# Kernel optimization log

Hardware: AMD Instinct MI355X
Metric: run time of the kernel (lower is better)

Reference implementation:

```python
import jax, jax.numpy as jnp
import numpy as np
import math

EPS = 1.1920929e-07  # torch F.rms_norm default eps = fp32 machine epsilon


def rms_norm(x):
    # normalize over last dim, no learned weight (matches F.rms_norm(x, (d,)))
    var = jnp.mean(jnp.square(x), axis=-1, keepdims=True)
    return x * jax.lax.rsqrt(var + EPS)


def rotary(x, cos, sin):
    # x: (B, T, H, D); cos/sin: (T, D) -> broadcast over B, H
    d2 = x.shape[-1] // 2
    x1, x2 = x[..., :d2], x[..., d2:]
    rot = jnp.concatenate([-x2, x1], axis=-1)  # rotate_half
    c = cos[None, :, None, :]
    s = sin[None, :, None, :]
    return x * c + rot * s


def setup_inputs() -> dict:
    key = jax.random.key(0)
    ks = jax.random.split(key, 5)
    B, T, C, H = 2, 2048, 1024, 16
    D = C // H
    x = jax.random.normal(ks[0], (B, T, C), dtype=jnp.float32)
    # real RoPE tables (theta=10000), duplicated across the two halves
    inv_freq = 1.0 / (10000.0 ** (np.arange(0, D, 2, dtype=np.float32) / D))
    pos = np.arange(T, dtype=np.float32)
    freqs = np.outer(pos, inv_freq)            # (T, D/2)
    emb = np.concatenate([freqs, freqs], -1)   # (T, D)
    cos = jnp.asarray(np.cos(emb), dtype=jnp.float32)
    sin = jnp.asarray(np.sin(emb), dtype=jnp.float32)
    sc_in = 1.0 / math.sqrt(C)
    W_attn = jax.random.normal(ks[1], (C, 3 * C), dtype=jnp.float32) * sc_in
    b_attn = jax.random.normal(ks[2], (3 * C,), dtype=jnp.float32) * 0.02
    W_proj = jax.random.normal(ks[3], (C, C), dtype=jnp.float32) * sc_in
    b_proj = jax.random.normal(ks[4], (C,), dtype=jnp.float32) * 0.02
    return {"x": x, "cos": cos, "sin": sin, "W_attn": W_attn, "b_attn": b_attn,
            "W_proj": W_proj, "b_proj": b_proj}


def reference(x, cos, sin, W_attn, b_attn, W_proj, b_proj):
    B, T, C = x.shape
    H = 16
    D = C // H
    qkv = x @ W_attn + b_attn                         # (B, T, 3C)
    qkv = qkv.reshape(B, T, 3, H, D)                  # 'b t (a h d) -> ...'
    q, k, v = qkv[:, :, 0], qkv[:, :, 1], qkv[:, :, 2]  # (B, T, H, D)
    q, k = rms_norm(q), rms_norm(k)
    q = rotary(q, cos, sin)
    k = rotary(k, cos, sin)
    # causal SDPA, scale = 1/sqrt(D)
    scale = 1.0 / math.sqrt(D)
    scores = jnp.einsum('bthd,bshd->bhts', q, k) * scale  # (B, H, T, T)
    causal = jnp.tril(jnp.ones((T, T), dtype=bool))
    scores = jnp.where(causal[None, None], scores, jnp.finfo(scores.dtype).min)
    attn = jax.nn.softmax(scores, axis=-1)
    y = jnp.einsum('bhts,bshd->bthd', attn, v)            # (B, T, H, D)
    y = y.reshape(B, T, C)
    return y @ W_proj + b_proj
```

## Files before the change

kernel.cpp:

```cpp
#include <hip/hip_runtime.h>
#include <math.h>

#define EPSV 1.1920929e-07f

typedef __attribute__((ext_vector_type(8))) short short8;
typedef __attribute__((ext_vector_type(4))) float f32x4;

__device__ __forceinline__ float bf2f(unsigned short u) {
    union { unsigned int i; float f; } c; c.i = ((unsigned int)u) << 16; return c.f;
}
__device__ __forceinline__ unsigned short f2bf(float f) {
    union { float f; unsigned int i; } c; c.f = f;
    unsigned int r = c.i + 0x7FFFu + ((c.i >> 16) & 1u);
    return (unsigned short)(r >> 16);
}
__device__ __forceinline__ unsigned int pack_bf16_ru(float a, float b) {
    union { float f; unsigned int i; } ca, cb; ca.f = a; cb.f = b;
    return __builtin_amdgcn_perm(cb.i + 0x8000u, ca.i + 0x8000u, 0x07060302u);
}
__device__ __forceinline__ void async_lds16(const unsigned short* g, unsigned short* l) {
    __builtin_amdgcn_global_load_lds(
        (const __attribute__((address_space(1))) unsigned int*)g,
        (__attribute__((address_space(3))) unsigned int*)l, 16, 0, 0);
}

__global__ __launch_bounds__(256) void cast_bf16(
    const float* __restrict__ src, unsigned short* __restrict__ dst, int n)
{
    const int i = (blockIdx.x * 256 + threadIdx.x) * 4;
    if (i >= n) return;
    const float4 v = *(const float4*)&src[i];
    ushort4 o;
    o.x = f2bf(v.x); o.y = f2bf(v.y); o.z = f2bf(v.z); o.w = f2bf(v.w);
    *(ushort4*)&dst[i] = o;
}

__global__ __launch_bounds__(256) void transpose_cast_both(
    const float* __restrict__ Wa, unsigned short* __restrict__ Wat,
    const float* __restrict__ Wp, unsigned short* __restrict__ Wpt)
{
    __shared__ float tile[32][33];
    int bx = blockIdx.x;
    const float* W; unsigned short* Wt; int N;
    if (bx < 96) { W = Wa; Wt = Wat; N = 3072; }
    else         { W = Wp; Wt = Wpt; N = 1024; bx -= 96; }
    const int n0 = bx * 32, k0 = blockIdx.y * 32;
    const int r = threadIdx.x >> 3, c4 = (threadIdx.x & 7) * 4;
    const float4 v = *(const float4*)&W[(size_t)(k0 + r) * N + n0 + c4];
    tile[r][c4 + 0] = v.x; tile[r][c4 + 1] = v.y;
    tile[r][c4 + 2] = v.z; tile[r][c4 + 3] = v.w;
    __syncthreads();
    ushort4 o;
    o.x = f2bf(tile[c4 + 0][r]); o.y = f2bf(tile[c4 + 1][r]);
    o.z = f2bf(tile[c4 + 2][r]); o.w = f2bf(tile[c4 + 3][r]);
    *(ushort4*)&Wt[(size_t)(n0 + r) * 1024 + k0 + c4] = o;
}

template <bool OUT_BF16>
__global__ __launch_bounds__(256) void gemm_bf16(
    const unsigned short* __restrict__ A,
    const unsigned short* __restrict__ Bt,
    const float* __restrict__ bias,
    void* __restrict__ Cv,
    int M, int N, int K)
{
    __shared__ unsigned short As0[128][32], As1[128][32];
    __shared__ unsigned short Bs0[128][32], Bs1[128][32];
    const int t    = threadIdx.x;
    const int lane = t & 63;
    const int wv   = t >> 6;
    const int wrow = (wv >> 1) * 64;
    const int wcol = (wv & 1) * 64;
    const int m0 = blockIdx.y * 128;
    const int n0 = blockIdx.x * 128;
    const int col  = lane & 15;
    const int quad = lane >> 4;

    const int srow = (wv << 5) + (lane >> 2);
    const int scol = (lane & 3) << 3;
    const unsigned short* a00 = A  + (size_t)(m0 + srow) * K + scol;
    const unsigned short* a10 = a00 + (size_t)16 * K;
    const unsigned short* a01 = a00 + 32;
    const unsigned short* a11 = a10 + 32;
    const unsigned short* b00 = Bt + (size_t)(n0 + srow) * K + scol;
    const unsigned short* b10 = b00 + (size_t)16 * K;
    const unsigned short* b01 = b00 + 32;
    const unsigned short* b11 = b10 + 32;
    unsigned short* al0 = &As0[srow][scol];
    unsigned short* al1 = &As0[srow + 16][scol];
    unsigned short* al2 = &As1[srow][scol];
    unsigned short* al3 = &As1[srow + 16][scol];
    unsigned short* bl0 = &Bs0[srow][scol];
    unsigned short* bl1 = &Bs0[srow + 16][scol];
    unsigned short* bl2 = &Bs1[srow][scol];
    unsigned short* bl3 = &Bs1[srow + 16][scol];

    f32x4 acc[4][4];
    #pragma unroll
    for (int i = 0; i < 4; ++i)
        #pragma unroll
        for (int j = 0; j < 4; ++j)
            acc[i][j] = (f32x4){0.f, 0.f, 0.f, 0.f};

    for (int k0 = 0; k0 < K; k0 += 64) {
        async_lds16(a00, al0);
        async_lds16(a10, al1);
        async_lds16(a01, al2);
        async_lds16(a11, al3);
        async_lds16(b00, bl0);
        async_lds16(b10, bl1);
        async_lds16(b01, bl2);
        async_lds16(b11, bl3);
        a00 += 64; a10 += 64; a01 += 64; a11 += 64;
        b00 += 64; b10 += 64; b01 += 64; b11 += 64;
        __syncthreads();
        short8 af[2][4], bf[2][4];
        #pragma unroll
        for (int mt = 0; mt < 4; ++mt) {
            af[0][mt] = *(const short8*)&As0[wrow + mt * 16 + col][quad << 3];
            af[1][mt] = *(const short8*)&As1[wrow + mt * 16 + col][quad << 3];
        }
        #pragma unroll
        for (int nt = 0; nt < 4; ++nt) {
            bf[0][nt] = *(const short8*)&Bs0[wcol + nt * 16 + col][quad << 3];
            bf[1][nt] = *(const short8*)&Bs1[wcol + nt * 16 + col][quad << 3];
        }
        #pragma unroll
        for (int ks = 0; ks < 2; ++ks)
            #pragma unroll
            for (int mt = 0; mt < 4; ++mt)
                #pragma unroll
                for (int nt = 0; nt < 4; ++nt)
                    acc[mt][nt] = __builtin_amdgcn_mfma_f32_16x16x32_bf16(
                        af[ks][mt], bf[ks][nt], acc[mt][nt], 0, 0, 0);
        __syncthreads();
    }

    const int rowq = quad << 2;
    #pragma unroll
    for (int nt = 0; nt < 4; ++nt) {
        const int n = n0 + wcol + nt * 16 + col;
        const float bv = bias[n];
        #pragma unroll
        for (int mt = 0; mt < 4; ++mt) {
            #pragma unroll
            for (int r = 0; r < 4; ++r) {
                const int m = m0 + wrow + mt * 16 + rowq + r;
                const float v = acc[mt][nt][r] + bv;
                if (OUT_BF16)
                    ((unsigned short*)Cv)[(size_t)m * N + n] = f2bf(v);
                else
                    ((float*)Cv)[(size_t)m * N + n] = v;
            }
        }
    }
}

__global__ __launch_bounds__(256) void gemm_bf16_n64(
    const unsigned short* __restrict__ A,
    const unsigned short* __restrict__ Bt,
    const float* __restrict__ bias,
    float* __restrict__ C,
    int M, int N, int K)
{
    __shared__ unsigned short As0[128][32], As1[128][32];
    __shared__ unsigned short Bs0[64][32], Bs1[64][32];
    const int t    = threadIdx.x;
    const int lane = t & 63;
    const int wv   = t >> 6;
    const int wrow = wv << 5;
    const int m0 = blockIdx.y * 128;
    const int n0 = blockIdx.x * 64;
    const int col  = lane & 15;
    const int quad = lane >> 4;

    const int srow = (wv << 5) + (lane >> 2);
    const int scol = (lane & 3) << 3;
    const unsigned short* a00 = A  + (size_t)(m0 + srow) * K + scol;
    const unsigned short* a10 = a00 + (size_t)16 * K;
    const unsigned short* a01 = a00 + 32;
    const unsigned short* a11 = a10 + 32;
    const int bsrow = (wv << 4) + (lane >> 2);
    const unsigned short* b00 = Bt + (size_t)(n0 + bsrow) * K + scol;
    const unsigned short* b01 = b00 + 32;
    unsigned short* al0 = &As0[srow][scol];
    unsigned short* al1 = &As0[srow + 16][scol];
    unsigned short* al2 = &As1[srow][scol];
    unsigned short* al3 = &As1[srow + 16][scol];
    unsigned short* bl0 = &Bs0[bsrow][scol];
    unsigned short* bl1 = &Bs1[bsrow][scol];

    f32x4 acc[2][4];
    #pragma unroll
    for (int i = 0; i < 2; ++i)
        #pragma unroll
        for (int j = 0; j < 4; ++j)
            acc[i][j] = (f32x4){0.f, 0.f, 0.f, 0.f};

    for (int k0 = 0; k0 < K; k0 += 64) {
        async_lds16(a00, al0);
        async_lds16(a10, al1);
        async_lds16(a01, al2);
        async_lds16(a11, al3);
        async_lds16(b00, bl0);
        async_lds16(b01, bl1);
        a00 += 64; a10 += 64; a01 += 64; a11 += 64;
        b00 += 64; b01 += 64;
        __syncthreads();
        short8 af[2][2], bf[2][4];
        #pragma unroll
        for (int mt = 0; mt < 2; ++mt) {
            af[0][mt] = *(const short8*)&As0[wrow + mt * 16 + col][quad << 3];
            af[1][mt] = *(const short8*)&As1[wrow + mt * 16 + col][quad << 3];
        }
        #pragma unroll
        for (int nt = 0; nt < 4; ++nt) {
            bf[0][nt] = *(const short8*)&Bs0[nt * 16 + col][quad << 3];
            bf[1][nt] = *(const short8*)&Bs1[nt * 16 + col][quad << 3];
        }
        #pragma unroll
        for (int ks = 0; ks < 2; ++ks)
            #pragma unroll
            for (int mt = 0; mt < 2; ++mt)
                #pragma unroll
                for (int nt = 0; nt < 4; ++nt)
                    acc[mt][nt] = __builtin_amdgcn_mfma_f32_16x16x32_bf16(
                        af[ks][mt], bf[ks][nt], acc[mt][nt], 0, 0, 0);
        __syncthreads();
    }

    const int rowq = quad << 2;
    #pragma unroll
    for (int nt = 0; nt < 4; ++nt) {
        const int n = n0 + nt * 16 + col;
        const float bv = bias[n];
        #pragma unroll
        for (int mt = 0; mt < 2; ++mt) {
            #pragma unroll
            for (int r = 0; r < 4; ++r) {
                const int m = m0 + wrow + mt * 16 + rowq + r;
                C[(size_t)m * N + n] = acc[mt][nt][r] + bv;
            }
        }
    }
}

__global__ __launch_bounds__(256) void rmsnorm_rope(
    unsigned short* __restrict__ qkv, const float* __restrict__ cosp,
    const float* __restrict__ sinp, int BT, int T)
{
    const int wid  = (blockIdx.x << 2) + (threadIdx.x >> 6);
    const int lane = threadIdx.x & 63;
    const int hq = wid & 3;
    const int w  = (wid >> 2) & 1;
    const int bt = wid >> 3;
    if (bt >= BT) return;
    const int h  = (hq << 2) + (lane >> 4);
    const int d4 = (lane & 15) << 2;
    const int tpos = bt % T;
    const size_t idx = (size_t)bt * 3072 + (w << 10) + (h << 6) + d4;

    const ushort4 u = *(const ushort4*)&qkv[idx];
    const float x0 = bf2f(u.x), x1 = bf2f(u.y), x2 = bf2f(u.z), x3 = bf2f(u.w);
    float ss = x0 * x0 + x1 * x1 + x2 * x2 + x3 * x3;
    ss += __shfl_xor(ss, 1, 64);
    ss += __shfl_xor(ss, 2, 64);
    ss += __shfl_xor(ss, 4, 64);
    ss += __shfl_xor(ss, 8, 64);
    const float rn = rsqrtf(ss * (1.0f / 64.0f) + EPSV);
    const float xn0 = x0 * rn, xn1 = x1 * rn, xn2 = x2 * rn, xn3 = x3 * rn;
    const float p0 = __shfl_xor(xn0, 8, 64);
    const float p1 = __shfl_xor(xn1, 8, 64);
    const float p2 = __shfl_xor(xn2, 8, 64);
    const float p3 = __shfl_xor(xn3, 8, 64);
    const float sgn = (d4 < 32) ? -1.0f : 1.0f;
    const float4 c = *(const float4*)&cosp[tpos * 64 + d4];
    const float4 s = *(const float4*)&sinp[tpos * 64 + d4];
    const float scale = (w == 0) ? 0.18033688011112042f : 1.0f;
    ushort4 o;
    o.x = f2bf(fmaf(xn0, c.x, sgn * p0 * s.x) * scale);
    o.y = f2bf(fmaf(xn1, c.y, sgn * p1 * s.y) * scale);
    o.z = f2bf(fmaf(xn2, c.z, sgn * p2 * s.z) * scale);
    o.w = f2bf(fmaf(xn3, c.w, sgn * p3 * s.w) * scale);
    *(ushort4*)&qkv[idx] = o;
}

__global__ __launch_bounds__(256) void v_transpose(
    const unsigned short* __restrict__ qkv, unsigned short* __restrict__ vt,
    int T)
{
    __shared__ unsigned short tile[64][72];
    const int bh = blockIdx.x;
    const int b  = bh >> 4, h = bh & 15;
    const int t0 = blockIdx.y << 6;
    const int t  = threadIdx.x;
    const unsigned short* vbase = qkv + (size_t)b * T * 3072 + 2048 + (h << 6);

    #pragma unroll
    for (int i = 0; i < 2; ++i) {
        const int c = t + (i << 8);
        const int r = c >> 3, c8 = (c & 7) << 3;
        const short8 v = *(const short8*)&vbase[(size_t)(t0 + r) * 3072 + c8];
        #pragma unroll
        for (int j = 0; j < 8; ++j)
            tile[c8 + j][r] = (unsigned short)v[j];
    }
    __syncthreads();
    #pragma unroll
    for (int i = 0; i < 2; ++i) {
        const int c = t + (i << 8);
        const int d = c >> 3, c8 = (c & 7) << 3;
        const short8 o = *(const short8*)&tile[d][c8];
        *(short8*)&vt[((size_t)bh * 64 + d) * T + t0 + c8] = o;
    }
}

__global__ __launch_bounds__(256, 2) void flash_attn_mfma(
    const unsigned short* __restrict__ qkv,
    const unsigned short* __restrict__ vt,
    unsigned short* __restrict__ yb,
    int B, int T)
{
    const int bh = blockIdx.x;
    const int b  = bh >> 4, h = bh & 15;
    const int ny = (int)gridDim.y;
    const int y  = (int)blockIdx.y;
    const int hny = (ny + 1) >> 1;
    const int jq = (y < hny) ? (ny - 1 - y) : (y - hny);
    const int q0 = jq << 7;
    const int t  = threadIdx.x;
    const int lane = t & 63;
    const int w    = t >> 6;
    const int col  = lane & 15;
    const int quad = lane >> 4;

    __shared__ unsigned short Kb[2][64][64];
    __shared__ unsigned short Vb[2][64][64];
    __shared__ unsigned short Ps[4][32][72];

    const unsigned short* qb  = qkv + (size_t)b * T * 3072 + (h << 6);
    const unsigned short* kb  = qb + 1024;
    const unsigned short* vtb = vt + (size_t)bh * 64 * T;

    const int qw  = q0 + (w << 5);
    const int qg0 = qw + col;
    const int qg1 = qw + 16 + col;

    short8 qf[2][2];
    {
        const unsigned short* qrow0 = qb + (size_t)qg0 * 3072 + (quad << 3);
        qf[0][0] = *(const short8*)&qrow0[0];
        qf[0][1] = *(const short8*)&qrow0[32];
        const unsigned short* qrow1 = qb + (size_t)qg1 * 3072 + (quad << 3);
        qf[1][0] = *(const short8*)&qrow1[0];
        qf[1][1] = *(const short8*)&qrow1[32];
    }

    f32x4 oacc[2][4];
    #pragma unroll
    for (int qc = 0; qc < 2; ++qc)
        #pragma unroll
        for (int i = 0; i < 4; ++i) oacc[qc][i] = (f32x4){0.f, 0.f, 0.f, 0.f};
    float l_i[2] = {0.f, 0.f};

    const int sr = t >> 3;
    const int sg = (((t & 7) ^ (sr & 7)) << 3);
    const unsigned short* kp0 = kb  + (size_t)sr * 3072 + sg;
    const unsigned short* kp1 = kb  + (size_t)(sr + 32) * 3072 + sg;
    const unsigned short* vp0 = vtb + (size_t)sr * T + sg;
    const unsigned short* vp1 = vtb + (size_t)(sr + 32) * T + sg;

    {
        unsigned short* kd = &Kb[0][0][0] + (t << 3);
        unsigned short* vd = &Vb[0][0][0] + (t << 3);
        async_lds16(kp0, kd);
        async_lds16(kp1, kd + 2048);
        async_lds16(vp0, vd);
        async_lds16(vp1, vd + 2048);
        kp0 += (size_t)64 * 3072; kp1 += (size_t)64 * 3072;
        vp0 += 64; vp1 += 64;
    }

    const int cs0 = ((quad ^ (col & 7)) << 3);
    const int cs1 = (((4 + quad) ^ (col & 7)) << 3);

    const int last_kt = (q0 + 127) >> 6;
    int cur = 0;
    for (int kt = 0; kt <= last_kt; ++kt) {
        const int k0 = kt << 6;
        __syncthreads();
        if (kt < last_kt) {
            unsigned short* kd = &Kb[cur ^ 1][0][0] + (t << 3);
            unsigned short* vd = &Vb[cur ^ 1][0][0] + (t << 3);
            async_lds16(kp0, kd);
            async_lds16(kp1, kd + 2048);
            async_lds16(vp0, vd);
            async_lds16(vp1, vd + 2048);
            kp0 += (size_t)64 * 3072; kp1 += (size_t)64 * 3072;
            vp0 += 64; vp1 += 64;
        }

        if (k0 <= qw + 31) {
            const unsigned short (*Kc)[64] = Kb[cur];
            const unsigned short (*Vc)[64] = Vb[cur];

            f32x4 st[2][4];
            #pragma unroll
            for (int qc = 0; qc < 2; ++qc)
                #pragma unroll
                for (int i = 0; i < 4; ++i) st[qc][i] = (f32x4){0.f, 0.f, 0.f, 0.f};
            __builtin_amdgcn_s_setprio(1);
            #pragma unroll
            for (int ks = 0; ks < 2; ++ks)
                #pragma unroll
                for (int mt = 0; mt < 4; ++mt) {
                    const short8 kf = *(const short8*)&Kc[mt * 16 + col][ks ? cs1 : cs0];
                    st[0][mt] = __builtin_amdgcn_mfma_f32_16x16x32_bf16(kf, qf[0][ks], st[0][mt], 0, 0, 0);
                    st[1][mt] = __builtin_amdgcn_mfma_f32_16x16x32_bf16(kf, qf[1][ks], st[1][mt], 0, 0, 0);
                }
            __builtin_amdgcn_s_setprio(0);

            #pragma unroll
            for (int qc = 0; qc < 2; ++qc) {
                const int qg = qw + (qc << 4) + col;
                const bool diag = (k0 + 63 > qw + (qc << 4));
                unsigned short* pw = &Ps[w][(qc << 4) + col][0];
                float rs = 0.f;
                #pragma unroll
                for (int mt = 0; mt < 4; ++mt) {
                    float x0 = st[qc][mt][0], x1 = st[qc][mt][1];
                    float x2 = st[qc][mt][2], x3 = st[qc][mt][3];
                    if (diag) {
                        const int sbase = k0 + mt * 16 + (quad << 2);
                        if (sbase + 0 > qg) x0 = -INFINITY;
                        if (sbase + 1 > qg) x1 = -INFINITY;
                        if (sbase + 2 > qg) x2 = -INFINITY;
                        if (sbase + 3 > qg) x3 = -INFINITY;
                    }
                    const float p0 = __builtin_amdgcn_exp2f(x0);
                    const float p1 = __builtin_amdgcn_exp2f(x1);
                    const float p2 = __builtin_amdgcn_exp2f(x2);
                    const float p3 = __builtin_amdgcn_exp2f(x3);
                    rs += (p0 + p1) + (p2 + p3);
                    uint2 pk;
                    pk.x = pack_bf16_ru(p0, p1);
                    pk.y = pack_bf16_ru(p2, p3);
                    *(uint2*)&pw[mt * 16 + (quad << 2)] = pk;
                }
                rs += __shfl_xor(rs, 16, 64);
                rs += __shfl_xor(rs, 32, 64);
                l_i[qc] += rs;
            }

            __builtin_amdgcn_s_setprio(1);
            #pragma unroll
            for (int ks = 0; ks < 2; ++ks) {
                const short8 pf0 = *(const short8*)&Ps[w][col][ks * 32 + (quad << 3)];
                const short8 pf1 = *(const short8*)&Ps[w][16 + col][ks * 32 + (quad << 3)];
                #pragma unroll
                for (int mt = 0; mt < 4; ++mt) {
                    const short8 vf = *(const short8*)&Vc[mt * 16 + col][ks ? cs1 : cs0];
                    oacc[0][mt] = __builtin_amdgcn_mfma_f32_16x16x32_bf16(vf, pf0, oacc[0][mt], 0, 0, 0);
                    oacc[1][mt] = __builtin_amdgcn_mfma_f32_16x16x32_bf16(vf, pf1, oacc[1][mt], 0, 0, 0);
                }
            }
            __builtin_amdgcn_s_setprio(0);
        }
        cur ^= 1;
    }

    const float inv0 = 1.0f / l_i[0];
    const float inv1 = 1.0f / l_i[1];
    unsigned short* yrow0 = yb + (size_t)(b * T + qg0) * 1024 + (h << 6);
    unsigned short* yrow1 = yb + (size_t)(b * T + qg1) * 1024 + (h << 6);
    #pragma unroll
    for (int mt = 0; mt < 4; ++mt) {
        ushort4 yv0, yv1;
        yv0.x = f2bf(oacc[0][mt][0] * inv0);
        yv0.y = f2bf(oacc[0][mt][1] * inv0);
        yv0.z = f2bf(oacc[0][mt][2] * inv0);
        yv0.w = f2bf(oacc[0][mt][3] * inv0);
        yv1.x = f2bf(oacc[1][mt][0] * inv1);
        yv1.y = f2bf(oacc[1][mt][1] * inv1);
        yv1.z = f2bf(oacc[1][mt][2] * inv1);
        yv1.w = f2bf(oacc[1][mt][3] * inv1);
        *(ushort4*)&yrow0[mt * 16 + (quad << 2)] = yv0;
        *(ushort4*)&yrow1[mt * 16 + (quad << 2)] = yv1;
    }
}

extern "C" void kernel_launch(void* const* d_in, const int* in_sizes, int n_in,
                              void* d_out, int out_size, void* d_ws, size_t ws_size,
                              hipStream_t stream)
{
    const float* x      = (const float*)d_in[0];
    const float* cosp   = (const float*)d_in[1];
    const float* sinp   = (const float*)d_in[2];
    const float* W_attn = (const float*)d_in[3];
    const float* b_attn = (const float*)d_in[4];
    const float* W_proj = (const float*)d_in[5];
    const float* b_proj = (const float*)d_in[6];
    float* out = (float*)d_out;

    const int C = 1024, H = 16;
    const int T  = in_sizes[1] / 64;
    const int BT = in_sizes[0] / C;
    const int B  = BT / T;

    unsigned short* qkvb = (unsigned short*)d_ws;
    unsigned short* xb   = qkvb + (size_t)BT * 3072;
    unsigned short* Wab  = xb   + (size_t)BT * 1024;
    unsigned short* Wpb  = Wab  + (size_t)3072 * 1024;
    unsigned short* yb   = Wpb  + (size_t)1024 * 1024;
    unsigned short* vtb  = xb;

    cast_bf16<<<dim3(BT * C / 1024), dim3(256), 0, stream>>>(x, xb, BT * C);
    transpose_cast_both<<<dim3(128, 32), dim3(256), 0, stream>>>(
        W_attn, Wab, W_proj, Wpb);

    gemm_bf16<true><<<dim3(3 * C / 128, BT / 128), dim3(256), 0, stream>>>(
        xb, Wab, b_attn, qkvb, BT, 3 * C, C);

    rmsnorm_rope<<<dim3(BT * 2), dim3(256), 0, stream>>>(
        qkvb, cosp, sinp, BT, T);

    v_transpose<<<dim3(B * H, T / 64), dim3(256), 0, stream>>>(qkvb, vtb, T);

    flash_attn_mfma<<<dim3(B * H, T / 128), dim3(256), 0, stream>>>(
        qkvb, vtb, yb, B, T);

    gemm_bf16_n64<<<dim3(C / 64, BT / 128), dim3(256), 0, stream>>>(
        yb, Wpb, b_proj, out, BT, C, C);
}
```

Measured before the change: 206.2 us.

## Split flash attention KV loop across two wave groups with LDS reduction

Doubles the attention block to 512 threads. Each pair of waves shares a 32-row query slice, and the two waves split the KV tiles by parity. At the end, partial O accumulators and row sums are combined through shared memory before normalisation. The goal is more parallelism per query tile and better latency hiding, at the cost of idle waves on alternate tiles, an extra reduction step and higher LDS use.

```diff
diff --git a/kernel.cpp b/kernel.cpp
--- a/kernel.cpp
+++ b/kernel.cpp
@@ -315,7 +315,7 @@
     }
 }
 
-__global__ __launch_bounds__(256, 2) void flash_attn_mfma(
+__global__ __launch_bounds__(512, 4) void flash_attn_mfma(
     const unsigned short* __restrict__ qkv,
     const unsigned short* __restrict__ vt,
     unsigned short* __restrict__ yb,
@@ -331,18 +331,21 @@
     const int t  = threadIdx.x;
     const int lane = t & 63;
     const int w    = t >> 6;
+    const int qg   = w >> 1;
+    const int sp   = w & 1;
     const int col  = lane & 15;
     const int quad = lane >> 4;
 
-    __shared__ unsigned short Kb[2][64][64];
-    __shared__ unsigned short Vb[2][64][64];
-    __shared__ unsigned short Ps[4][32][72];
+    __shared__ __align__(16) unsigned short smem[34816];
+    unsigned short* Kb = smem;
+    unsigned short* Vb = smem + 8192;
+    unsigned short* Ps = smem + 16384;
 
     const unsigned short* qb  = qkv + (size_t)b * T * 3072 + (h << 6);
     const unsigned short* kb  = qb + 1024;
     const unsigned short* vtb = vt + (size_t)bh * 64 * T;
 
-    const int qw  = q0 + (w << 5);
+    const int qw  = q0 + (qg << 5);
     const int qg0 = qw + col;
     const int qg1 = qw + 16 + col;
 
@@ -365,21 +368,12 @@
 
     const int sr = t >> 3;
     const int sg = (((t & 7) ^ (sr & 7)) << 3);
-    const unsigned short* kp0 = kb  + (size_t)sr * 3072 + sg;
-    const unsigned short* kp1 = kb  + (size_t)(sr + 32) * 3072 + sg;
-    const unsigned short* vp0 = vtb + (size_t)sr * T + sg;
-    const unsigned short* vp1 = vtb + (size_t)(sr + 32) * T + sg;
-
-    {
-        unsigned short* kd = &Kb[0][0][0] + (t << 3);
-        unsigned short* vd = &Vb[0][0][0] + (t << 3);
-        async_lds16(kp0, kd);
-        async_lds16(kp1, kd + 2048);
-        async_lds16(vp0, vd);
-        async_lds16(vp1, vd + 2048);
-        kp0 += (size_t)64 * 3072; kp1 += (size_t)64 * 3072;
-        vp0 += 64; vp1 += 64;
-    }
+    const unsigned short* kp = kb  + (size_t)sr * 3072 + sg;
+    const unsigned short* vp = vtb + (size_t)sr * T + sg;
+
+    async_lds16(kp, Kb + (t << 3));
+    async_lds16(vp, Vb + (t << 3));
+    kp += (size_t)64 * 3072; vp += 64;
 
     const int cs0 = ((quad ^ (col & 7)) << 3);
     const int cs1 = (((4 + quad) ^ (col & 7)) << 3);
@@ -390,19 +384,14 @@
         const int k0 = kt << 6;
         __syncthreads();
         if (kt < last_kt) {
-            unsigned short* kd = &Kb[cur ^ 1][0][0] + (t << 3);
-            unsigned short* vd = &Vb[cur ^ 1][0][0] + (t << 3);
-            async_lds16(kp0, kd);
-            async_lds16(kp1, kd + 2048);
-            async_lds16(vp0, vd);
-            async_lds16(vp1, vd + 2048);
-            kp0 += (size_t)64 * 3072; kp1 += (size_t)64 * 3072;
-            vp0 += 64; vp1 += 64;
-        }
-
-        if (k0 <= qw + 31) {
-            const unsigned short (*Kc)[64] = Kb[cur];
-            const unsigned short (*Vc)[64] = Vb[cur];
+            async_lds16(kp, Kb + ((cur ^ 1) << 12) + (t << 3));
+            async_lds16(vp, Vb + ((cur ^ 1) << 12) + (t << 3));
+            kp += (size_t)64 * 3072; vp += 64;
+        }
+
+        if (((kt & 1) == sp) && (k0 <= qw + 31)) {
+            const unsigned short* Kc = Kb + (cur << 12);
+            const unsigned short* Vc = Vb + (cur << 12);
 
             f32x4 st[2][4];
             #pragma unroll
@@ -414,7 +403,7 @@
             for (int ks = 0; ks < 2; ++ks)
                 #pragma unroll
                 for (int mt = 0; mt < 4; ++mt) {
-                    const short8 kf = *(const short8*)&Kc[mt * 16 + col][ks ? cs1 : cs0];
+                    const short8 kf = *(const short8*)&Kc[(mt * 16 + col) * 64 + (ks ? cs1 : cs0)];
                     st[0][mt] = __builtin_amdgcn_mfma_f32_16x16x32_bf16(kf, qf[0][ks], st[0][mt], 0, 0, 0);
                     st[1][mt] = __builtin_amdgcn_mfma_f32_16x16x32_bf16(kf, qf[1][ks], st[1][mt], 0, 0, 0);
                 }
@@ -422,9 +411,9 @@
 
             #pragma unroll
             for (int qc = 0; qc < 2; ++qc) {
-                const int qg = qw + (qc << 4) + col;
+                const int qg_ = qw + (qc << 4) + col;
                 const bool diag = (k0 + 63 > qw + (qc << 4));
-                unsigned short* pw = &Ps[w][(qc << 4) + col][0];
+                unsigned short* pw = Ps + ((w << 5) + (qc << 4) + col) * 72;
                 float rs = 0.f;
                 #pragma unroll
                 for (int mt = 0; mt < 4; ++mt) {
@@ -432,10 +421,10 @@
                     float x2 = st[qc][mt][2], x3 = st[qc][mt][3];
                     if (diag) {
                         const int sbase = k0 + mt * 16 + (quad << 2);
-                        if (sbase + 0 > qg) x0 = -INFINITY;
-                        if (sbase + 1 > qg) x1 = -INFINITY;
-                        if (sbase + 2 > qg) x2 = -INFINITY;
-                        if (sbase + 3 > qg) x3 = -INFINITY;
+                        if (sbase + 0 > qg_) x0 = -INFINITY;
+                        if (sbase + 1 > qg_) x1 = -INFINITY;
+                        if (sbase + 2 > qg_) x2 = -INFINITY;
+                        if (sbase + 3 > qg_) x3 = -INFINITY;
                     }
                     const float p0 = __builtin_amdgcn_exp2f(x0);
                     const float p1 = __builtin_amdgcn_exp2f(x1);
@@ -455,11 +444,11 @@
             __builtin_amdgcn_s_setprio(1);
             #pragma unroll
             for (int ks = 0; ks < 2; ++ks) {
-                const short8 pf0 = *(const short8*)&Ps[w][col][ks * 32 + (quad << 3)];
-                const short8 pf1 = *(const short8*)&Ps[w][16 + col][ks * 32 + (quad << 3)];
+                const short8 pf0 = *(const short8*)&Ps[((w << 5) + col) * 72 + ks * 32 + (quad << 3)];
+                const short8 pf1 = *(const short8*)&Ps[((w << 5) + 16 + col) * 72 + ks * 32 + (quad << 3)];
                 #pragma unroll
                 for (int mt = 0; mt < 4; ++mt) {
-                    const short8 vf = *(const short8*)&Vc[mt * 16 + col][ks ? cs1 : cs0];
+                    const short8 vf = *(const short8*)&Vc[(mt * 16 + col) * 64 + (ks ? cs1 : cs0)];
                     oacc[0][mt] = __builtin_amdgcn_mfma_f32_16x16x32_bf16(vf, pf0, oacc[0][mt], 0, 0, 0);
                     oacc[1][mt] = __builtin_amdgcn_mfma_f32_16x16x32_bf16(vf, pf1, oacc[1][mt], 0, 0, 0);
                 }
@@ -469,23 +458,44 @@
         cur ^= 1;
     }
 
-    const float inv0 = 1.0f / l_i[0];
-    const float inv1 = 1.0f / l_i[1];
-    unsigned short* yrow0 = yb + (size_t)(b * T + qg0) * 1024 + (h << 6);
-    unsigned short* yrow1 = yb + (size_t)(b * T + qg1) * 1024 + (h << 6);
-    #pragma unroll
-    for (int mt = 0; mt < 4; ++mt) {
-        ushort4 yv0, yv1;
-        yv0.x = f2bf(oacc[0][mt][0] * inv0);
-        yv0.y = f2bf(oacc[0][mt][1] * inv0);
-        yv0.z = f2bf(oacc[0][mt][2] * inv0);
-        yv0.w = f2bf(oacc[0][mt][3] * inv0);
-        yv1.x = f2bf(oacc[1][mt][0] * inv1);
-        yv1.y = f2bf(oacc[1][mt][1] * inv1);
-        yv1.z = f2bf(oacc[1][mt][2] * inv1);
-        yv1.w = f2bf(oacc[1][mt][3] * inv1);
-        *(ushort4*)&yrow0[mt * 16 + (quad << 2)] = yv0;
-        *(ushort4*)&yrow1[mt * 16 + (quad << 2)] = yv1;
+    __syncthreads();
+    float* Of = (float*)smem;
+    float* Lf = ((float*)smem) + 9216;
+    if (sp) {
+        float* orow = Of + (((qg << 6) + lane) * 36);
+        #pragma unroll
+        for (int qc = 0; qc < 2; ++qc)
+            #pragma unroll
+            for (int mt = 0; mt < 4; ++mt)
+                *(f32x4*)&orow[(qc << 4) + (mt << 2)] = oacc[qc][mt];
+        if (quad == 0) {
+            Lf[(qg << 5) + col] = l_i[0];
+            Lf[(qg << 5) + 16 + col] = l_i[1];
+        }
+    }
+    __syncthreads();
+    if (!sp) {
+        const float* orow = Of + (((qg << 6) + lane) * 36);
+        const float inv0 = 1.0f / (l_i[0] + Lf[(qg << 5) + col]);
+        const float inv1 = 1.0f / (l_i[1] + Lf[(qg << 5) + 16 + col]);
+        unsigned short* yrow0 = yb + (size_t)(b * T + qg0) * 1024 + (h << 6);
+        unsigned short* yrow1 = yb + (size_t)(b * T + qg1) * 1024 + (h << 6);
+        #pragma unroll
+        for (int mt = 0; mt < 4; ++mt) {
+            const f32x4 p0 = *(const f32x4*)&orow[(mt << 2)];
+            const f32x4 p1 = *(const f32x4*)&orow[16 + (mt << 2)];
+            ushort4 yv0, yv1;
+            yv0.x = f2bf((oacc[0][mt][0] + p0[0]) * inv0);
+            yv0.y = f2bf((oacc[0][mt][1] + p0[1]) * inv0);
+            yv0.z = f2bf((oacc[0][mt][2] + p0[2]) * inv0);
+            yv0.w = f2bf((oacc[0][mt][3] + p0[3]) * inv0);
+            yv1.x = f2bf((oacc[1][mt][0] + p1[0]) * inv1);
+            yv1.y = f2bf((oacc[1][mt][1] + p1[1]) * inv1);
+            yv1.z = f2bf((oacc[1][mt][2] + p1[2]) * inv1);
+            yv1.w = f2bf((oacc[1][mt][3] + p1[3]) * inv1);
+            *(ushort4*)&yrow0[mt * 16 + (quad << 2)] = yv0;
+            *(ushort4*)&yrow1[mt * 16 + (quad << 2)] = yv1;
+        }
     }
 }
 
@@ -526,7 +536,7 @@
 
     v_transpose<<<dim3(B * H, T / 64), dim3(256), 0, stream>>>(qkvb, vtb, T);
 
-    flash_attn_mfma<<<dim3(B * H, T / 128), dim3(256), 0, stream>>>(
+    flash_attn_mfma<<<dim3(B * H, T / 128), dim3(512), 0, stream>>>(
         qkvb, vtb, yb, B, T);
 
     gemm_bf16_n64<<<dim3(C / 64, BT / 128), dim3(256), 0, stream>>>(
```

Measured after the change: 212.5 us. 3.0% more time.
